# Performance work log

Hardware: AMD Instinct MI355X
Metric: run time of the kernel (lower is better)

Reference implementation:

```python
import jax, jax.numpy as jnp
from jax import lax
import numpy as np

CONF_THRESH = 0.015
NMS_DIST = 4
BORDER = 4
RED = 8


def setup_inputs() -> dict:
    key = jax.random.key(0)
    k1, k2, k3, k4, k5 = jax.random.split(key, 5)
    B, C, H, W = 32, 128, 64, 64
    MID, NCLS = 256, RED * RED + 1
    return {
        "x": jax.random.normal(k1, (B, C, H, W), dtype=jnp.float32),
        "w1": jax.random.normal(k2, (MID, C, 3, 3), dtype=jnp.float32) * 0.05,
        "b1": jax.random.normal(k3, (MID,), dtype=jnp.float32) * 0.05,
        "w2": jax.random.normal(k4, (NCLS, MID, 1, 1), dtype=jnp.float32) * 0.05,
        "b2": jax.random.normal(k5, (NCLS,), dtype=jnp.float32) * 0.05,
    }


def _conv3x3(x, w, b):
    y = lax.conv_general_dilated(
        x, w, window_strides=(1, 1), padding="SAME",
        dimension_numbers=("NCHW", "OIHW", "NCHW"))
    return y + b[None, :, None, None]


def _max_pool(s, r):
    # s: [B, H, W]; infinity-norm neighborhood max, window (2r+1)x(2r+1)
    return lax.reduce_window(
        s, -jnp.inf, lax.max,
        window_dimensions=(1, 2 * r + 1, 2 * r + 1),
        window_strides=(1, 1, 1), padding="SAME")


def _grid_nms(scores, r, iters=8):
    # Iterated local-max suppression; converges to the greedy (sorted-by-score)
    # grid NMS of the original nms_fast routine for distinct scores.
    zeros = jnp.zeros_like(scores)
    max_mask = (scores == _max_pool(scores, r)) & (scores > 0)
    for _ in range(iters):
        supp = _max_pool(max_mask.astype(scores.dtype), r) > 0
        supp_scores = jnp.where(supp, zeros, scores)
        new_max = (supp_scores == _max_pool(supp_scores, r)) & (supp_scores > 0)
        max_mask = max_mask | (new_max & ~supp)
    return jnp.where(max_mask, scores, zeros)


def reference(x, w1, b1, w2, b2):
    B, _, hh, ww = x.shape
    h = jax.nn.relu(_conv3x3(x, w1, b1))                       # [B, mid, hh, ww]
    semi = jnp.einsum("bchw,oc->bohw", h, w2[:, :, 0, 0]) + b2[None, :, None, None]
    dense = jax.nn.softmax(semi, axis=1)                        # [B, 65, hh, ww]
    nodust = dense[:, :-1]                                      # drop dust bin
    # depth-to-space: [B,64,hh,ww] -> [B, hh*8, ww*8]
    heat = nodust.transpose(0, 2, 3, 1).reshape(B, hh, ww, RED, RED)
    heat = heat.transpose(0, 1, 3, 2, 4).reshape(B, hh * RED, ww * RED)
    # confidence threshold
    scores = jnp.where(heat >= CONF_THRESH, heat, 0.0)
    # grid-based NMS (dense keep-map formulation of nms_fast)
    kept = _grid_nms(scores, NMS_DIST)
    # border removal
    Hi, Wi = hh * RED, ww * RED
    yy = jnp.arange(Hi)
    xx = jnp.arange(Wi)
    border = ((yy[:, None] >= BORDER) & (yy[:, None] < Hi - BORDER) &
              (xx[None, :] >= BORDER) & (xx[None, :] < Wi - BORDER))
    return kept * border[None, :, :].astype(kept.dtype)
```

## Files before the change

### kernel.cpp

```cpp
#include <hip/hip_runtime.h>
#include <hip/hip_bf16.h>
#include <stdint.h>

#define BATCH 32
#define CIN 128
#define HH 64
#define WW 64
#define MID 256
#define NCLS 65
#define HI 512
#define NWORDS 8
#define HBS2 264
#define SEMS 68
#define RMS 68

typedef _Float16 half8 __attribute__((ext_vector_type(8)));
typedef _Float16 half4v __attribute__((ext_vector_type(4)));
typedef _Float16 half2v __attribute__((ext_vector_type(2)));
typedef float f32x4 __attribute__((ext_vector_type(4)));

__global__ __launch_bounds__(256) void prep_w1f(
    const float* __restrict__ w1, _Float16* __restrict__ w1fh,
    _Float16* __restrict__ w1fl)
{
    const int idx = blockIdx.x * 256 + threadIdx.x;
    const int j = idx & 7, lane = (idx >> 3) & 63, mt = (idx >> 9) & 15;
    const int s = (idx >> 13) & 3, kix = idx >> 15;
    const int m = mt * 16 + (lane & 15);
    const int c = s * 32 + (lane >> 4) * 8 + j;
    const int ky = kix / 3, kx = kix - ky * 3;
    const float v = w1[((m * CIN + c) * 3 + ky) * 3 + kx];
    const _Float16 hi = (_Float16)v;
    w1fh[idx] = hi;
    w1fl[idx] = (_Float16)(v - (float)hi);
}

__global__ __launch_bounds__(256) void prep_w2f(
    const float* __restrict__ w2, _Float16* __restrict__ w2fh,
    _Float16* __restrict__ w2fl)
{
    const int idx = blockIdx.x * 256 + threadIdx.x;
    const int j = idx & 7, lane = (idx >> 3) & 63;
    const int ks = (idx >> 9) & 7, mt = idx >> 12;
    const int o = mt * 16 + (lane & 15);
    const int k = ks * 32 + (lane >> 4) * 8 + j;
    const float v = (o < NCLS) ? w2[o * MID + k] : 0.f;
    const _Float16 hi = (_Float16)v;
    w2fh[idx] = hi;
    w2fl[idx] = (_Float16)(v - (float)hi);
}

__global__ __launch_bounds__(256, 3) void head_kernel(
    const float* __restrict__ x,
    const _Float16* __restrict__ w1fh, const _Float16* __restrict__ w1fl,
    const _Float16* __restrict__ w2fh, const _Float16* __restrict__ w2fl,
    const float* __restrict__ b1, const float* __restrict__ b2,
    float* __restrict__ out)
{
    const int b  = blockIdx.z;
    const int y0 = blockIdx.y * 8, x0 = blockIdx.x * 8;
    const int tid = threadIdx.x;
    const int lane = tid & 63, w = tid >> 6;
    const int n = lane & 15, q = lane >> 4;

    __shared__ __align__(16) unsigned char SM[51200];
    char* const xhb = (char*)SM;
    _Float16* const hbh = (_Float16*)SM;
    _Float16* const hbl = hbh + 32 * HBS2;
    float* const sem  = (float*)(SM + 33792);
    float* const rinv = sem + 32 * SEMS;

    const float* xb = x + (size_t)b * CIN * HH * WW;
    for (int i = tid; i < 6400; i += 256) {
        const int c2 = i / 100, pos = i - c2 * 100;
        const int r = pos / 10, cc = pos - r * 10;
        const int gy = y0 - 1 + r, gx = x0 - 1 + cc;
        float v0 = 0.f, v1 = 0.f;
        if ((unsigned)gy < HH && (unsigned)gx < WW) {
            const float* p = xb + (c2 * 2 * HH + gy) * WW + gx;
            v0 = p[0]; v1 = p[HH * WW];
        }
        const _Float16 h0 = (_Float16)v0, h1 = (_Float16)v1;
        half2v hi = {h0, h1};
        half2v lo = {(_Float16)(v0 - (float)h0), (_Float16)(v1 - (float)h1)};
        const int slot = (c2 >> 2) ^ (pos & 15);
        char* p16 = xhb + pos * 256 + (slot << 4) + (c2 & 3) * 4;
        *(half2v*)p16 = hi;
        *(half2v*)(p16 + 25600) = lo;
    }
    __syncthreads();

    f32x4 acc[4][4];
#pragma unroll
    for (int i = 0; i < 4; ++i)
#pragma unroll
        for (int t = 0; t < 4; ++t) acc[i][t] = (f32x4){0.f, 0.f, 0.f, 0.f};

    int bposT[4];
#pragma unroll
    for (int t = 0; t < 4; ++t)
        bposT[t] = (t * 2 + (n >> 3)) * 10 + (n & 7);

    for (int kix = 0; kix < 9; ++kix) {
        const int ky = kix / 3;
        const int koff = ky * 10 + (kix - ky * 3);
#pragma unroll
        for (int s = 0; s < 4; ++s) {
            half8 Bh[4], Bl[4];
#pragma unroll
            for (int t = 0; t < 4; ++t) {
                const int pos = bposT[t] + koff;
                const int byteoff = pos * 256 +
                    ((((s << 2) + q) ^ (pos & 15)) << 4);
                Bh[t] = *(const half8*)(xhb + byteoff);
                Bl[t] = *(const half8*)(xhb + 25600 + byteoff);
            }
#pragma unroll
            for (int i = 0; i < 4; ++i) {
                const size_t o = (size_t)(kix * 4 + s) * 8192 +
                                 (w * 4 + i) * 512 + lane * 8;
                const half8 Ah = *(const half8*)(w1fh + o);
                const half8 Al = *(const half8*)(w1fl + o);
#pragma unroll
                for (int t = 0; t < 4; ++t) {
                    acc[i][t] = __builtin_amdgcn_mfma_f32_16x16x32_f16(
                        Ah, Bh[t], acc[i][t], 0, 0, 0);
                    acc[i][t] = __builtin_amdgcn_mfma_f32_16x16x32_f16(
                        Ah, Bl[t], acc[i][t], 0, 0, 0);
                    acc[i][t] = __builtin_amdgcn_mfma_f32_16x16x32_f16(
                        Al, Bh[t], acc[i][t], 0, 0, 0);
                }
            }
        }
    }
    __syncthreads();

    for (int hf = 0; hf < 2; ++hf) {
        if (hf) __syncthreads();
#pragma unroll
        for (int i = 0; i < 4; ++i)
#pragma unroll
            for (int tt = 0; tt < 2; ++tt) {
                const int t = hf * 2 + tt;
                const int p = tt * 16 + n;
                const int m0 = w * 64 + i * 16 + q * 4;
                const f32x4 a = acc[i][t];
                const float4 bv = *(const float4*)(b1 + m0);
                const float h0 = fmaxf(a[0] + bv.x, 0.f);
                const float h1 = fmaxf(a[1] + bv.y, 0.f);
                const float h2 = fmaxf(a[2] + bv.z, 0.f);
                const float h3 = fmaxf(a[3] + bv.w, 0.f);
                half4v hh = {(_Float16)h0, (_Float16)h1,
                             (_Float16)h2, (_Float16)h3};
                half4v hl = {(_Float16)(h0 - (float)hh[0]),
                             (_Float16)(h1 - (float)hh[1]),
                             (_Float16)(h2 - (float)hh[2]),
                             (_Float16)(h3 - (float)hh[3])};
                *(half4v*)(hbh + p * HBS2 + m0) = hh;
                *(half4v*)(hbl + p * HBS2 + m0) = hl;
            }
        __syncthreads();
        {
            const int nt = w & 1;
            const int mt0 = (w < 2) ? 0 : 3;
            const int nmt = (w < 2) ? 3 : 2;
            const int pb = nt * 16 + n;
            f32x4 a2[3];
#pragma unroll
            for (int j = 0; j < 3; ++j) a2[j] = (f32x4){0.f, 0.f, 0.f, 0.f};
#pragma unroll
            for (int ks = 0; ks < 8; ++ks) {
                const int ad = pb * HBS2 + ks * 32 + q * 8;
                const half8 B2h = *(const half8*)(hbh + ad);
                const half8 B2l = *(const half8*)(hbl + ad);
#pragma unroll
                for (int j = 0; j < 3; ++j)
                    if (j < nmt) {
                        const size_t o = (size_t)((mt0 + j) * 8 + ks) * 512 +
                                         lane * 8;
                        const half8 A2h = *(const half8*)(w2fh + o);
                        const half8 A2l = *(const half8*)(w2fl + o);
                        a2[j] = __builtin_amdgcn_mfma_f32_16x16x32_f16(
                            A2h, B2h, a2[j], 0, 0, 0);
                        a2[j] = __builtin_amdgcn_mfma_f32_16x16x32_f16(
                            A2h, B2l, a2[j], 0, 0, 0);
                        a2[j] = __builtin_amdgcn_mfma_f32_16x16x32_f16(
                            A2l, B2h, a2[j], 0, 0, 0);
                    }
            }
#pragma unroll
            for (int j = 0; j < 3; ++j)
                if (j < nmt) {
                    const int o0 = (mt0 + j) * 16 + q * 4;
#pragma unroll
                    for (int r2 = 0; r2 < 4; ++r2) {
                        const int o = o0 + r2;
                        if (o < NCLS)
                            sem[pb * SEMS + o] = a2[j][r2] + b2[o];
                    }
                }
        }
        __syncthreads();
        if (tid < 128) {
            const int p = tid >> 2, q4 = tid & 3;
            const int o0 = q4 * 17;
            const int o1 = (o0 + 17 < NCLS) ? o0 + 17 : NCLS;
            float mx = -1e30f;
            for (int o = o0; o < o1; ++o)
                mx = fmaxf(mx, sem[p * SEMS + o]);
            mx = fmaxf(mx, __shfl_xor(mx, 1));
            mx = fmaxf(mx, __shfl_xor(mx, 2));
            float ssum = 0.f;
            for (int o = o0; o < o1; ++o) {
                float e = __expf(sem[p * SEMS + o] - mx);
                sem[p * SEMS + o] = e;
                ssum += e;
            }
            ssum += __shfl_xor(ssum, 1);
            ssum += __shfl_xor(ssum, 2);
            if (q4 == 0) rinv[p] = 1.f / ssum;
        }
        __syncthreads();
        for (int t2 = tid; t2 < 2048; t2 += 256) {
            const int p = t2 >> 6, o = t2 & 63;
            float v = sem[p * SEMS + o] * rinv[p];
            if (!(v >= 0.015f)) v = 0.f;
            const int P = hf * 32 + p;
            const int py = P >> 3, px = P & 7;
            const int row = (y0 + py) * 8 + (o >> 3);
            const int col = (x0 + px) * 8 + (o & 7);
            out[((size_t)b * HI + row) * HI + col] = v;
        }
    }
}

__global__ __launch_bounds__(256, 8) void nms_iter(
    const float* __restrict__ S, const uint64_t* __restrict__ Min,
    uint64_t* __restrict__ Mout)
{
    const int b = blockIdx.z;
    const int bx = blockIdx.x;
    const int ty = blockIdx.y * 64, tx = bx * 64;
    const int tid = threadIdx.x;

    __shared__ uint64_t smw[80 * 3];
    __shared__ uint64_t hd[80 * 3];
    __shared__ uint64_t sup[72 * 3];
    __shared__ __align__(16) float rm[40 * RMS];

    if (tid < 240) {
        const int i = tid / 3, j = tid % 3;
        const int yy = ty - 8 + i;
        const int wj = bx - 1 + j;
        uint64_t v = 0;
        if (Min && (unsigned)yy < HI && (unsigned)wj < NWORDS)
            v = Min[((size_t)b * HI + yy) * NWORDS + wj];
        smw[tid] = v;
    }
    __syncthreads();
    if (tid < 240) {
        const int j = tid % 3;
        const uint64_t c = smw[tid];
        const uint64_t l = j > 0 ? smw[tid - 1] : 0ull;
        const uint64_t r = j < 2 ? smw[tid + 1] : 0ull;
        uint64_t d = c;
#pragma unroll
        for (int s = 1; s <= 4; ++s)
            d |= (c >> s) | (r << (64 - s)) | (c << s) | (l >> (64 - s));
        hd[tid] = d;
    }
    __syncthreads();
    if (tid < 216) {
        uint64_t v = 0;
#pragma unroll
        for (int k = 0; k < 9; ++k) v |= hd[tid + 3 * k];
        sup[tid] = v;
    }
    __syncthreads();

    const float* Sb = S + (size_t)b * HI * HI;
    for (int half = 0; half < 2; ++half) {
        const int rbase = half * 32;
        for (int k = tid; k < 640; k += 256) {
            const int rr = k >> 4, g = k & 15;
            const int r = rbase + rr;
            const int gy = ty - 4 + r;
            const int x4 = g * 4;
            const int gx0 = tx + x4 - 4;
            float v[12];
            if ((unsigned)gy < HI) {
                const float* row = Sb + (size_t)gy * HI;
                if (gx0 >= 0 && gx0 <= HI - 12) {
                    const float4 A  = *(const float4*)(row + gx0);
                    const float4 Bq = *(const float4*)(row + gx0 + 4);
                    const float4 Cq = *(const float4*)(row + gx0 + 8);
                    v[0]=A.x; v[1]=A.y; v[2]=A.z; v[3]=A.w;
                    v[4]=Bq.x; v[5]=Bq.y; v[6]=Bq.z; v[7]=Bq.w;
                    v[8]=Cq.x; v[9]=Cq.y; v[10]=Cq.z; v[11]=Cq.w;
                } else {
#pragma unroll
                    for (int cc = 0; cc < 12; ++cc)
                        v[cc] = ((unsigned)(gx0 + cc) < HI) ? row[gx0 + cc]
                                                            : 0.f;
                }
            } else {
#pragma unroll
                for (int cc = 0; cc < 12; ++cc) v[cc] = 0.f;
            }
            const uint64_t* sr = sup + r * 3;
            const uint64_t w0 = sr[(60 + x4) >> 6];
            const uint64_t w1 = sr[(64 + x4) >> 6];
            const uint64_t w2 = sr[(68 + x4) >> 6];
            const int b0 = (60 + x4) & 63;
            const int b1 = (64 + x4) & 63;
            const int b2 = (68 + x4) & 63;
#pragma unroll
            for (int cc = 0; cc < 4; ++cc) {
                if ((w0 >> (b0 + cc)) & 1ull) v[cc] = 0.f;
                if ((w1 >> (b1 + cc)) & 1ull) v[4 + cc] = 0.f;
                if ((w2 >> (b2 + cc)) & 1ull) v[8 + cc] = 0.f;
            }
            const float m4567 = fmaxf(fmaxf(v[4],v[5]), fmaxf(v[6],v[7]));
            const float m23 = fmaxf(v[2],v[3]), m89 = fmaxf(v[8],v[9]);
            const float o0 = fmaxf(fmaxf(fmaxf(v[0],v[1]), m23),
                                   fmaxf(m4567, v[8]));
            const float o1 = fmaxf(fmaxf(v[1], m23), fmaxf(m4567, m89));
            const float o2 = fmaxf(fmaxf(m23, m4567), fmaxf(m89, v[10]));
            const float o3 = fmaxf(fmaxf(v[3], m4567),
                                   fmaxf(fmaxf(m89, v[10]), v[11]));
            *(float4*)(rm + rr * RMS + x4) = make_float4(o0,o1,o2,o3);
        }
        __syncthreads();
        {
            const int wv = tid >> 6, lane = tid & 63;
            const int rb = wv * 8;
            const int ybase = rbase + rb;
            float ring[9];
#pragma unroll
            for (int k = 0; k < 8; ++k) ring[k] = rm[(rb + k) * RMS + lane];
#pragma unroll
            for (int qq = 0; qq < 8; ++qq) {
                const int y = ybase + qq;
                ring[(qq + 8) % 9] = rm[(rb + qq + 8) * RMS + lane];
                float mv = ring[0];
#pragma unroll
                for (int k = 1; k < 9; ++k) mv = fmaxf(mv, ring[k]);
                float c = Sb[(size_t)(ty + y) * HI + tx + lane];
                if ((sup[(y + 4) * 3 + 1] >> lane) & 1ull) c = 0.f;
                const uint64_t oldw = smw[(y + 8) * 3 + 1];
                const bool keep = ((oldw >> lane) & 1ull) ||
                                  (c > 0.f && c == mv);
                const uint64_t word = __ballot(keep);
                if (lane == 0)
                    Mout[((size_t)b * HI + ty + y) * NWORDS + bx] = word;
            }
        }
        __syncthreads();
    }
}

__global__ __launch_bounds__(256) void finalize_bits(
    float* __restrict__ S, const uint64_t* __restrict__ Mw)
{
    const int i4 = blockIdx.x * 256 + threadIdx.x;
    const size_t base = (size_t)i4 * 4;
    const int x = (int)(base & 511);
    const int y = (int)((base >> 9) & 511);
    const int bb = (int)(base >> 18);
    const uint64_t w = Mw[((size_t)bb * HI + y) * NWORDS + (x >> 6)];
    float4 v = ((const float4*)S)[i4];
    float* pv = (float*)&v;
    const bool rowok = (y >= 4) && (y < HI - 4);
#pragma unroll
    for (int cc = 0; cc < 4; ++cc) {
        const int xx = x + cc;
        const bool keep = rowok && (xx >= 4) && (xx < HI - 4) &&
                          ((w >> (xx & 63)) & 1ull);
        if (!keep) pv[cc] = 0.f;
    }
    ((float4*)S)[i4] = v;
}

extern "C" void kernel_launch(void* const* d_in, const int* in_sizes, int n_in,
                              void* d_out, int out_size, void* d_ws, size_t ws_size,
                              hipStream_t stream) {
    const float* x  = (const float*)d_in[0];
    const float* w1 = (const float*)d_in[1];
    const float* b1 = (const float*)d_in[2];
    const float* w2 = (const float*)d_in[3];
    const float* b2 = (const float*)d_in[4];
    float* out = (float*)d_out;

    char* wsb = (char*)d_ws;
    _Float16* w1fh = (_Float16*)(wsb);
    _Float16* w1fl = (_Float16*)(wsb + 0x90000);
    _Float16* w2fh = (_Float16*)(wsb + 0x120000);
    _Float16* w2fl = (_Float16*)(wsb + 0x130000);
    uint64_t* MA   = (uint64_t*)(wsb + 0x140000);
    uint64_t* MB   = (uint64_t*)(wsb + 0x240000);

    prep_w1f<<<294912 / 256, 256, 0, stream>>>(w1, w1fh, w1fl);
    prep_w2f<<<20480 / 256, 256, 0, stream>>>(w2, w2fh, w2fl);
    head_kernel<<<dim3(8, 8, BATCH), 256, 0, stream>>>(
        x, w1fh, w1fl, w2fh, w2fl, b1, b2, out);

    dim3 g(NWORDS, 8, BATCH);
    nms_iter<<<g, 256, 0, stream>>>(out, nullptr, MA);
    for (int it = 0; it < 4; ++it) {
        nms_iter<<<g, 256, 0, stream>>>(out, MA, MB);
        nms_iter<<<g, 256, 0, stream>>>(out, MB, MA);
    }
    const int nf4 = BATCH * HI * HI / 4;
    finalize_bits<<<nf4 / 256, 256, 0, stream>>>(out, MA);
}
```

Measured before the change: 536.0 us.

## Fuse pairs of NMS iterations per launch and fold finalize into last pass

Adds an nms_pair kernel that computes two suppression iterations per launch using an enlarged halo tile in shared memory, halving the number of NMS launches from nine to five. When workspace allows, scores are written to a workspace buffer and a new nms_last kernel applies the final iteration, the border mask and the output write together, removing the separate finalize pass. This trades extra halo recomputation and larger shared memory (lower occupancy bound) for fewer launches and less global traffic.

Result: slower. 598.8 us (+11.7%).

```diff
diff --git a/kernel.cpp b/kernel.cpp
--- a/kernel.cpp
+++ b/kernel.cpp
@@ -234,7 +234,7 @@
     }
 }
 
-__global__ __launch_bounds__(256, 8) void nms_iter(
+__global__ __launch_bounds__(256, 4) void nms_pair(
     const float* __restrict__ S, const uint64_t* __restrict__ Min,
     uint64_t* __restrict__ Mout)
 {
@@ -243,17 +243,256 @@
     const int ty = blockIdx.y * 64, tx = bx * 64;
     const int tid = threadIdx.x;
 
+    __shared__ uint64_t smw[96 * 3];
+    __shared__ uint64_t hd[96 * 3];
+    __shared__ uint64_t sup[88 * 3];
+    __shared__ uint64_t mkA[80 * 3];
+    __shared__ __align__(16) float hm[88 * 80];
+
+    const float* Sb = S + (size_t)b * HI * HI;
+
+    for (int k = tid; k < 288; k += 256) {
+        const int i = k / 3, j = k - (k / 3) * 3;
+        const int yy = ty - 16 + i;
+        const int wj = bx - 1 + j;
+        uint64_t v = 0;
+        if (Min && (unsigned)yy < HI && (unsigned)wj < NWORDS)
+            v = Min[((size_t)b * HI + yy) * NWORDS + wj];
+        smw[k] = v;
+    }
+    __syncthreads();
+    for (int k = tid; k < 288; k += 256) {
+        const int j = k % 3;
+        const uint64_t c = smw[k];
+        const uint64_t l = j > 0 ? smw[k - 1] : 0ull;
+        const uint64_t r = j < 2 ? smw[k + 1] : 0ull;
+        uint64_t d = c;
+#pragma unroll
+        for (int s = 1; s <= 4; ++s)
+            d |= (c >> s) | (r << (64 - s)) | (c << s) | (l >> (64 - s));
+        hd[k] = d;
+    }
+    __syncthreads();
+    for (int k = tid; k < 264; k += 256) {
+        uint64_t v = 0;
+#pragma unroll
+        for (int t = 0; t < 9; ++t) v |= hd[k + 3 * t];
+        sup[k] = v;
+    }
+    __syncthreads();
+    for (int k = tid; k < 1760; k += 256) {
+        const int r = k / 20, g = k - (k / 20) * 20;
+        const int gy = ty - 12 + r;
+        const int gx0 = tx - 12 + 4 * g;
+        float v[12];
+        if ((unsigned)gy < HI) {
+            const float* row = Sb + (size_t)gy * HI;
+            if (gx0 >= 0 && gx0 <= HI - 12) {
+                const float4 A  = *(const float4*)(row + gx0);
+                const float4 Bq = *(const float4*)(row + gx0 + 4);
+                const float4 Cq = *(const float4*)(row + gx0 + 8);
+                v[0]=A.x; v[1]=A.y; v[2]=A.z; v[3]=A.w;
+                v[4]=Bq.x; v[5]=Bq.y; v[6]=Bq.z; v[7]=Bq.w;
+                v[8]=Cq.x; v[9]=Cq.y; v[10]=Cq.z; v[11]=Cq.w;
+            } else {
+#pragma unroll
+                for (int cc = 0; cc < 12; ++cc)
+                    v[cc] = ((unsigned)(gx0 + cc) < HI) ? row[gx0 + cc] : 0.f;
+            }
+        } else {
+#pragma unroll
+            for (int cc = 0; cc < 12; ++cc) v[cc] = 0.f;
+        }
+        const uint64_t* sr = sup + r * 3;
+        const int rb0 = 52 + 4 * g;
+        const uint64_t w0 = sr[rb0 >> 6];
+        const uint64_t w1 = sr[(rb0 + 4) >> 6];
+        const uint64_t w2 = sr[(rb0 + 8) >> 6];
+        const int b0 = rb0 & 63, b1 = (rb0 + 4) & 63, b2 = (rb0 + 8) & 63;
+#pragma unroll
+        for (int cc = 0; cc < 4; ++cc) {
+            if ((w0 >> (b0 + cc)) & 1ull) v[cc] = 0.f;
+            if ((w1 >> (b1 + cc)) & 1ull) v[4 + cc] = 0.f;
+            if ((w2 >> (b2 + cc)) & 1ull) v[8 + cc] = 0.f;
+        }
+        const float m4567 = fmaxf(fmaxf(v[4],v[5]), fmaxf(v[6],v[7]));
+        const float m23 = fmaxf(v[2],v[3]), m89 = fmaxf(v[8],v[9]);
+        const float o0 = fmaxf(fmaxf(fmaxf(v[0],v[1]), m23),
+                               fmaxf(m4567, v[8]));
+        const float o1 = fmaxf(fmaxf(v[1], m23), fmaxf(m4567, m89));
+        const float o2 = fmaxf(fmaxf(m23, m4567), fmaxf(m89, v[10]));
+        const float o3 = fmaxf(fmaxf(v[3], m4567),
+                               fmaxf(fmaxf(m89, v[10]), v[11]));
+        *(float4*)(hm + r * 80 + 4 * g) = make_float4(o0,o1,o2,o3);
+    }
+    __syncthreads();
+    {
+        const int wv = tid >> 6, lane = tid & 63;
+        const int a0 = wv * 20;
+        float ringA[9], ringB[9];
+#pragma unroll
+        for (int t = 0; t < 8; ++t) {
+            ringA[t] = hm[(a0 + t) * 80 + lane];
+            ringB[t] = (lane < 16) ? hm[(a0 + t) * 80 + 64 + lane] : 0.f;
+        }
+        for (int ii = 0; ii < 20; ++ii) {
+            const int a = a0 + ii;
+            ringA[(ii + 8) % 9] = hm[(a + 8) * 80 + lane];
+            ringB[(ii + 8) % 9] =
+                (lane < 16) ? hm[(a + 8) * 80 + 64 + lane] : 0.f;
+            float mvA = ringA[0], mvB = ringB[0];
+#pragma unroll
+            for (int t = 1; t < 9; ++t) {
+                mvA = fmaxf(mvA, ringA[t]);
+                mvB = fmaxf(mvB, ringB[t]);
+            }
+            const int gyA = ty - 8 + a;
+            const int colA = tx - 8 + lane;
+            float cA = 0.f;
+            if ((unsigned)gyA < HI && (unsigned)colA < HI)
+                cA = Sb[(size_t)gyA * HI + colA];
+            if ((sup[(a + 4) * 3 + ((56 + lane) >> 6)] >>
+                 ((56 + lane) & 63)) & 1ull)
+                cA = 0.f;
+            const bool bitA =
+                (smw[(a + 8) * 3 + ((56 + lane) >> 6)] >>
+                 ((56 + lane) & 63)) & 1ull;
+            const bool keepA = bitA || (cA > 0.f && cA == mvA);
+            bool keepB = false;
+            if (lane < 16) {
+                const int colB = tx + 56 + lane;
+                float cB = 0.f;
+                if ((unsigned)gyA < HI && (unsigned)colB < HI)
+                    cB = Sb[(size_t)gyA * HI + colB];
+                if ((sup[(a + 4) * 3 + ((120 + lane) >> 6)] >>
+                     ((120 + lane) & 63)) & 1ull)
+                    cB = 0.f;
+                const bool bitB =
+                    (smw[(a + 8) * 3 + ((120 + lane) >> 6)] >>
+                     ((120 + lane) & 63)) & 1ull;
+                keepB = bitB || (cB > 0.f && cB == mvB);
+            }
+            const uint64_t bA = __ballot(keepA);
+            const uint64_t bB = __ballot(keepB);
+            if (lane == 0) {
+                mkA[a * 3 + 0] = (bA & 0xFFull) << 56;
+                mkA[a * 3 + 1] = (bA >> 8) | ((bB & 0xFFull) << 56);
+                mkA[a * 3 + 2] = (bB >> 8) & 0xFFull;
+            }
+        }
+    }
+    __syncthreads();
+    for (int k = tid; k < 240; k += 256) {
+        const int j = k % 3;
+        const uint64_t c = mkA[k];
+        const uint64_t l = j > 0 ? mkA[k - 1] : 0ull;
+        const uint64_t r = j < 2 ? mkA[k + 1] : 0ull;
+        uint64_t d = c;
+#pragma unroll
+        for (int s = 1; s <= 4; ++s)
+            d |= (c >> s) | (r << (64 - s)) | (c << s) | (l >> (64 - s));
+        hd[k] = d;
+    }
+    __syncthreads();
+    for (int k = tid; k < 216; k += 256) {
+        uint64_t v = 0;
+#pragma unroll
+        for (int t = 0; t < 9; ++t) v |= hd[k + 3 * t];
+        sup[k] = v;
+    }
+    __syncthreads();
+    float* const rm = hm;
+    for (int k = tid; k < 1152; k += 256) {
+        const int r = k >> 4, g = k & 15;
+        const int gy = ty - 4 + r;
+        const int gx0 = tx + 4 * g - 4;
+        float v[12];
+        if ((unsigned)gy < HI) {
+            const float* row = Sb + (size_t)gy * HI;
+            if (gx0 >= 0 && gx0 <= HI - 12) {
+                const float4 A  = *(const float4*)(row + gx0);
+                const float4 Bq = *(const float4*)(row + gx0 + 4);
+                const float4 Cq = *(const float4*)(row + gx0 + 8);
+                v[0]=A.x; v[1]=A.y; v[2]=A.z; v[3]=A.w;
+                v[4]=Bq.x; v[5]=Bq.y; v[6]=Bq.z; v[7]=Bq.w;
+                v[8]=Cq.x; v[9]=Cq.y; v[10]=Cq.z; v[11]=Cq.w;
+            } else {
+#pragma unroll
+                for (int cc = 0; cc < 12; ++cc)
+                    v[cc] = ((unsigned)(gx0 + cc) < HI) ? row[gx0 + cc] : 0.f;
+            }
+        } else {
+#pragma unroll
+            for (int cc = 0; cc < 12; ++cc) v[cc] = 0.f;
+        }
+        const uint64_t* sr = sup + r * 3;
+        const int rb0 = 60 + 4 * g;
+        const uint64_t w0 = sr[rb0 >> 6];
+        const uint64_t w1 = sr[(rb0 + 4) >> 6];
+        const uint64_t w2 = sr[(rb0 + 8) >> 6];
+        const int b0 = rb0 & 63, b1 = (rb0 + 4) & 63, b2 = (rb0 + 8) & 63;
+#pragma unroll
+        for (int cc = 0; cc < 4; ++cc) {
+            if ((w0 >> (b0 + cc)) & 1ull) v[cc] = 0.f;
+            if ((w1 >> (b1 + cc)) & 1ull) v[4 + cc] = 0.f;
+            if ((w2 >> (b2 + cc)) & 1ull) v[8 + cc] = 0.f;
+        }
+        const float m4567 = fmaxf(fmaxf(v[4],v[5]), fmaxf(v[6],v[7]));
+        const float m23 = fmaxf(v[2],v[3]), m89 = fmaxf(v[8],v[9]);
+        const float o0 = fmaxf(fmaxf(fmaxf(v[0],v[1]), m23),
+                               fmaxf(m4567, v[8]));
+        const float o1 = fmaxf(fmaxf(v[1], m23), fmaxf(m4567, m89));
+        const float o2 = fmaxf(fmaxf(m23, m4567), fmaxf(m89, v[10]));
+        const float o3 = fmaxf(fmaxf(v[3], m4567),
+                               fmaxf(fmaxf(m89, v[10]), v[11]));
+        *(float4*)(rm + r * 68 + 4 * g) = make_float4(o0,o1,o2,o3);
+    }
+    __syncthreads();
+    {
+        const int wv = tid >> 6, lane = tid & 63;
+        const int y0w = wv * 16;
+        float ring[9];
+#pragma unroll
+        for (int t = 0; t < 8; ++t) ring[t] = rm[(y0w + t) * 68 + lane];
+        for (int ii = 0; ii < 16; ++ii) {
+            const int y = y0w + ii;
+            ring[(ii + 8) % 9] = rm[(y + 8) * 68 + lane];
+            float mv = ring[0];
+#pragma unroll
+            for (int t = 1; t < 9; ++t) mv = fmaxf(mv, ring[t]);
+            float c = Sb[(size_t)(ty + y) * HI + tx + lane];
+            if ((sup[(y + 4) * 3 + 1] >> lane) & 1ull) c = 0.f;
+            const bool old = (mkA[(y + 8) * 3 + 1] >> lane) & 1ull;
+            const bool keep = old || (c > 0.f && c == mv);
+            const uint64_t word = __ballot(keep);
+            if (lane == 0)
+                Mout[((size_t)b * HI + ty + y) * NWORDS + bx] = word;
+        }
+    }
+}
+
+__global__ __launch_bounds__(256, 8) void nms_last(
+    const float* __restrict__ S, const uint64_t* __restrict__ Min,
+    float* __restrict__ out)
+{
+    const int b = blockIdx.z;
+    const int bx = blockIdx.x;
+    const int ty = blockIdx.y * 64, tx = bx * 64;
+    const int tid = threadIdx.x;
+
     __shared__ uint64_t smw[80 * 3];
     __shared__ uint64_t hd[80 * 3];
     __shared__ uint64_t sup[72 * 3];
     __shared__ __align__(16) float rm[40 * RMS];
+
+    const float* Sb = S + (size_t)b * HI * HI;
 
     if (tid < 240) {
         const int i = tid / 3, j = tid % 3;
         const int yy = ty - 8 + i;
         const int wj = bx - 1 + j;
         uint64_t v = 0;
-        if (Min && (unsigned)yy < HI && (unsigned)wj < NWORDS)
+        if ((unsigned)yy < HI && (unsigned)wj < NWORDS)
             v = Min[((size_t)b * HI + yy) * NWORDS + wj];
         smw[tid] = v;
     }
@@ -278,7 +517,6 @@
     }
     __syncthreads();
 
-    const float* Sb = S + (size_t)b * HI * HI;
     for (int half = 0; half < 2; ++half) {
         const int rbase = half * 32;
         for (int k = tid; k < 640; k += 256) {
@@ -345,6 +583,135 @@
                 float mv = ring[0];
 #pragma unroll
                 for (int k = 1; k < 9; ++k) mv = fmaxf(mv, ring[k]);
+                const int gy = ty + y, gx = tx + lane;
+                const float corig = Sb[(size_t)gy * HI + gx];
+                float c = corig;
+                if ((sup[(y + 4) * 3 + 1] >> lane) & 1ull) c = 0.f;
+                const uint64_t oldw = smw[(y + 8) * 3 + 1];
+                const bool keep = ((oldw >> lane) & 1ull) ||
+                                  (c > 0.f && c == mv);
+                const bool border = (gy >= 4) && (gy < HI - 4) &&
+                                    (gx >= 4) && (gx < HI - 4);
+                out[((size_t)b * HI + gy) * HI + gx] =
+                    (keep && border) ? corig : 0.f;
+            }
+        }
+        __syncthreads();
+    }
+}
+
+__global__ __launch_bounds__(256, 8) void nms_iter(
+    const float* __restrict__ S, const uint64_t* __restrict__ Min,
+    uint64_t* __restrict__ Mout)
+{
+    const int b = blockIdx.z;
+    const int bx = blockIdx.x;
+    const int ty = blockIdx.y * 64, tx = bx * 64;
+    const int tid = threadIdx.x;
+
+    __shared__ uint64_t smw[80 * 3];
+    __shared__ uint64_t hd[80 * 3];
+    __shared__ uint64_t sup[72 * 3];
+    __shared__ __align__(16) float rm[40 * RMS];
+
+    const float* Sb = S + (size_t)b * HI * HI;
+
+    if (tid < 240) {
+        const int i = tid / 3, j = tid % 3;
+        const int yy = ty - 8 + i;
+        const int wj = bx - 1 + j;
+        uint64_t v = 0;
+        if (Min && (unsigned)yy < HI && (unsigned)wj < NWORDS)
+            v = Min[((size_t)b * HI + yy) * NWORDS + wj];
+        smw[tid] = v;
+    }
+    __syncthreads();
+    if (tid < 240) {
+        const int j = tid % 3;
+        const uint64_t c = smw[tid];
+        const uint64_t l = j > 0 ? smw[tid - 1] : 0ull;
+        const uint64_t r = j < 2 ? smw[tid + 1] : 0ull;
+        uint64_t d = c;
+#pragma unroll
+        for (int s = 1; s <= 4; ++s)
+            d |= (c >> s) | (r << (64 - s)) | (c << s) | (l >> (64 - s));
+        hd[tid] = d;
+    }
+    __syncthreads();
+    if (tid < 216) {
+        uint64_t v = 0;
+#pragma unroll
+        for (int k = 0; k < 9; ++k) v |= hd[tid + 3 * k];
+        sup[tid] = v;
+    }
+    __syncthreads();
+
+    for (int half = 0; half < 2; ++half) {
+        const int rbase = half * 32;
+        for (int k = tid; k < 640; k += 256) {
+            const int rr = k >> 4, g = k & 15;
+            const int r = rbase + rr;
+            const int gy = ty - 4 + r;
+            const int x4 = g * 4;
+            const int gx0 = tx + x4 - 4;
+            float v[12];
+            if ((unsigned)gy < HI) {
+                const float* row = Sb + (size_t)gy * HI;
+                if (gx0 >= 0 && gx0 <= HI - 12) {
+                    const float4 A  = *(const float4*)(row + gx0);
+                    const float4 Bq = *(const float4*)(row + gx0 + 4);
+                    const float4 Cq = *(const float4*)(row + gx0 + 8);
+                    v[0]=A.x; v[1]=A.y; v[2]=A.z; v[3]=A.w;
+                    v[4]=Bq.x; v[5]=Bq.y; v[6]=Bq.z; v[7]=Bq.w;
+                    v[8]=Cq.x; v[9]=Cq.y; v[10]=Cq.z; v[11]=Cq.w;
+                } else {
+#pragma unroll
+                    for (int cc = 0; cc < 12; ++cc)
+                        v[cc] = ((unsigned)(gx0 + cc) < HI) ? row[gx0 + cc]
+                                                            : 0.f;
+                }
+            } else {
+#pragma unroll
+                for (int cc = 0; cc < 12; ++cc) v[cc] = 0.f;
+            }
+            const uint64_t* sr = sup + r * 3;
+            const uint64_t w0 = sr[(60 + x4) >> 6];
+            const uint64_t w1 = sr[(64 + x4) >> 6];
+            const uint64_t w2 = sr[(68 + x4) >> 6];
+            const int b0 = (60 + x4) & 63;
+            const int b1 = (64 + x4) & 63;
+            const int b2 = (68 + x4) & 63;
+#pragma unroll
+            for (int cc = 0; cc < 4; ++cc) {
+                if ((w0 >> (b0 + cc)) & 1ull) v[cc] = 0.f;
+                if ((w1 >> (b1 + cc)) & 1ull) v[4 + cc] = 0.f;
+                if ((w2 >> (b2 + cc)) & 1ull) v[8 + cc] = 0.f;
+            }
+            const float m4567 = fmaxf(fmaxf(v[4],v[5]), fmaxf(v[6],v[7]));
+            const float m23 = fmaxf(v[2],v[3]), m89 = fmaxf(v[8],v[9]);
+            const float o0 = fmaxf(fmaxf(fmaxf(v[0],v[1]), m23),
+                                   fmaxf(m4567, v[8]));
+            const float o1 = fmaxf(fmaxf(v[1], m23), fmaxf(m4567, m89));
+            const float o2 = fmaxf(fmaxf(m23, m4567), fmaxf(m89, v[10]));
+            const float o3 = fmaxf(fmaxf(v[3], m4567),
+                                   fmaxf(fmaxf(m89, v[10]), v[11]));
+            *(float4*)(rm + rr * RMS + x4) = make_float4(o0,o1,o2,o3);
+        }
+        __syncthreads();
+        {
+            const int wv = tid >> 6, lane = tid & 63;
+            const int rb = wv * 8;
+            const int ybase = rbase + rb;
+            float ring[9];
+#pragma unroll
+            for (int k = 0; k < 8; ++k) ring[k] = rm[(rb + k) * RMS + lane];
+#pragma unroll
+            for (int qq = 0; qq < 8; ++qq) {
+                const int y = ybase + qq;
+                ring[(qq + 8) % 9] = rm[(rb + qq + 8) * RMS + lane];
+                float mv = ring[0];
+#pragma unroll
+                for (int k = 1; k < 9; ++k) mv = fmaxf(mv, ring[k]);
                 float c = Sb[(size_t)(ty + y) * HI + tx + lane];
                 if ((sup[(y + 4) * 3 + 1] >> lane) & 1ull) c = 0.f;
                 const uint64_t oldw = smw[(y + 8) * 3 + 1];
@@ -399,17 +766,27 @@
     uint64_t* MA   = (uint64_t*)(wsb + 0x140000);
     uint64_t* MB   = (uint64_t*)(wsb + 0x240000);
 
+    const size_t S_OFF = 0x340000;
+    const size_t S_BYTES = (size_t)BATCH * HI * HI * 4;
+    const bool use_ws = ws_size >= S_OFF + S_BYTES;
+    float* S = use_ws ? (float*)(wsb + S_OFF) : out;
+
     prep_w1f<<<294912 / 256, 256, 0, stream>>>(w1, w1fh, w1fl);
     prep_w2f<<<20480 / 256, 256, 0, stream>>>(w2, w2fh, w2fl);
     head_kernel<<<dim3(8, 8, BATCH), 256, 0, stream>>>(
-        x, w1fh, w1fl, w2fh, w2fl, b1, b2, out);
+        x, w1fh, w1fl, w2fh, w2fl, b1, b2, S);
 
     dim3 g(NWORDS, 8, BATCH);
-    nms_iter<<<g, 256, 0, stream>>>(out, nullptr, MA);
-    for (int it = 0; it < 4; ++it) {
-        nms_iter<<<g, 256, 0, stream>>>(out, MA, MB);
-        nms_iter<<<g, 256, 0, stream>>>(out, MB, MA);
-    }
-    const int nf4 = BATCH * HI * HI / 4;
-    finalize_bits<<<nf4 / 256, 256, 0, stream>>>(out, MA);
+    nms_pair<<<g, 256, 0, stream>>>(S, nullptr, MA);
+    nms_pair<<<g, 256, 0, stream>>>(S, MA, MB);
+    nms_pair<<<g, 256, 0, stream>>>(S, MB, MA);
+    nms_pair<<<g, 256, 0, stream>>>(S, MA, MB);
+
+    if (use_ws) {
+        nms_last<<<g, 256, 0, stream>>>(S, MB, out);
+    } else {
+        nms_iter<<<g, 256, 0, stream>>>(S, MB, MA);
+        const int nf4 = BATCH * HI * HI / 4;
+        finalize_bits<<<nf4 / 256, 256, 0, stream>>>(out, MA);
+    }
 }
```

## Fuse final NMS pass with border/finalize, merge weight prep kernels

Applied to the files above, without the earlier changes.

Merges the two weight-prep kernels into one launch. When the workspace is large enough, the head writes scores to a workspace buffer, and a new nms_last kernel runs the final suppression iteration and writes the masked, border-cleared scores straight to the output. This removes the separate finalize_bits pass over the full score map. The first NMS iteration also skips building the dilation bitmaps when there is no input mask. The cost is extra workspace use and a duplicated kernel body.

Result: faster. 524.1 us (-2.2%).

```diff
diff --git a/kernel.cpp b/kernel.cpp
--- a/kernel.cpp
+++ b/kernel.cpp
@@ -19,35 +19,33 @@
 typedef _Float16 half2v __attribute__((ext_vector_type(2)));
 typedef float f32x4 __attribute__((ext_vector_type(4)));
 
-__global__ __launch_bounds__(256) void prep_w1f(
-    const float* __restrict__ w1, _Float16* __restrict__ w1fh,
-    _Float16* __restrict__ w1fl)
+__global__ __launch_bounds__(256) void prep_wf(
+    const float* __restrict__ w1, const float* __restrict__ w2,
+    _Float16* __restrict__ w1fh, _Float16* __restrict__ w1fl,
+    _Float16* __restrict__ w2fh, _Float16* __restrict__ w2fl)
 {
     const int idx = blockIdx.x * 256 + threadIdx.x;
-    const int j = idx & 7, lane = (idx >> 3) & 63, mt = (idx >> 9) & 15;
-    const int s = (idx >> 13) & 3, kix = idx >> 15;
-    const int m = mt * 16 + (lane & 15);
-    const int c = s * 32 + (lane >> 4) * 8 + j;
-    const int ky = kix / 3, kx = kix - ky * 3;
-    const float v = w1[((m * CIN + c) * 3 + ky) * 3 + kx];
-    const _Float16 hi = (_Float16)v;
-    w1fh[idx] = hi;
-    w1fl[idx] = (_Float16)(v - (float)hi);
-}
-
-__global__ __launch_bounds__(256) void prep_w2f(
-    const float* __restrict__ w2, _Float16* __restrict__ w2fh,
-    _Float16* __restrict__ w2fl)
-{
-    const int idx = blockIdx.x * 256 + threadIdx.x;
-    const int j = idx & 7, lane = (idx >> 3) & 63;
-    const int ks = (idx >> 9) & 7, mt = idx >> 12;
-    const int o = mt * 16 + (lane & 15);
-    const int k = ks * 32 + (lane >> 4) * 8 + j;
-    const float v = (o < NCLS) ? w2[o * MID + k] : 0.f;
-    const _Float16 hi = (_Float16)v;
-    w2fh[idx] = hi;
-    w2fl[idx] = (_Float16)(v - (float)hi);
+    if (idx < 294912) {
+        const int j = idx & 7, lane = (idx >> 3) & 63, mt = (idx >> 9) & 15;
+        const int s = (idx >> 13) & 3, kix = idx >> 15;
+        const int m = mt * 16 + (lane & 15);
+        const int c = s * 32 + (lane >> 4) * 8 + j;
+        const int ky = kix / 3, kx = kix - ky * 3;
+        const float v = w1[((m * CIN + c) * 3 + ky) * 3 + kx];
+        const _Float16 hi = (_Float16)v;
+        w1fh[idx] = hi;
+        w1fl[idx] = (_Float16)(v - (float)hi);
+    } else {
+        const int i2 = idx - 294912;
+        const int j = i2 & 7, lane = (i2 >> 3) & 63;
+        const int ks = (i2 >> 9) & 7, mt = i2 >> 12;
+        const int o = mt * 16 + (lane & 15);
+        const int k = ks * 32 + (lane >> 4) * 8 + j;
+        const float v = (o < NCLS) ? w2[o * MID + k] : 0.f;
+        const _Float16 hi = (_Float16)v;
+        w2fh[i2] = hi;
+        w2fl[i2] = (_Float16)(v - (float)hi);
+    }
 }
 
 __global__ __launch_bounds__(256, 3) void head_kernel(
@@ -248,37 +246,44 @@
     __shared__ uint64_t sup[72 * 3];
     __shared__ __align__(16) float rm[40 * RMS];
 
-    if (tid < 240) {
-        const int i = tid / 3, j = tid % 3;
-        const int yy = ty - 8 + i;
-        const int wj = bx - 1 + j;
-        uint64_t v = 0;
-        if (Min && (unsigned)yy < HI && (unsigned)wj < NWORDS)
-            v = Min[((size_t)b * HI + yy) * NWORDS + wj];
-        smw[tid] = v;
-    }
-    __syncthreads();
-    if (tid < 240) {
-        const int j = tid % 3;
-        const uint64_t c = smw[tid];
-        const uint64_t l = j > 0 ? smw[tid - 1] : 0ull;
-        const uint64_t r = j < 2 ? smw[tid + 1] : 0ull;
-        uint64_t d = c;
-#pragma unroll
-        for (int s = 1; s <= 4; ++s)
-            d |= (c >> s) | (r << (64 - s)) | (c << s) | (l >> (64 - s));
-        hd[tid] = d;
-    }
-    __syncthreads();
-    if (tid < 216) {
-        uint64_t v = 0;
-#pragma unroll
-        for (int k = 0; k < 9; ++k) v |= hd[tid + 3 * k];
-        sup[tid] = v;
-    }
-    __syncthreads();
-
     const float* Sb = S + (size_t)b * HI * HI;
+
+    if (Min) {
+        if (tid < 240) {
+            const int i = tid / 3, j = tid % 3;
+            const int yy = ty - 8 + i;
+            const int wj = bx - 1 + j;
+            uint64_t v = 0;
+            if ((unsigned)yy < HI && (unsigned)wj < NWORDS)
+                v = Min[((size_t)b * HI + yy) * NWORDS + wj];
+            smw[tid] = v;
+        }
+        __syncthreads();
+        if (tid < 240) {
+            const int j = tid % 3;
+            const uint64_t c = smw[tid];
+            const uint64_t l = j > 0 ? smw[tid - 1] : 0ull;
+            const uint64_t r = j < 2 ? smw[tid + 1] : 0ull;
+            uint64_t d = c;
+#pragma unroll
+            for (int s = 1; s <= 4; ++s)
+                d |= (c >> s) | (r << (64 - s)) | (c << s) | (l >> (64 - s));
+            hd[tid] = d;
+        }
+        __syncthreads();
+        if (tid < 216) {
+            uint64_t v = 0;
+#pragma unroll
+            for (int k = 0; k < 9; ++k) v |= hd[tid + 3 * k];
+            sup[tid] = v;
+        }
+        __syncthreads();
+    } else {
+        if (tid < 240) smw[tid] = 0;
+        if (tid < 216) sup[tid] = 0;
+        __syncthreads();
+    }
+
     for (int half = 0; half < 2; ++half) {
         const int rbase = half * 32;
         for (int k = tid; k < 640; k += 256) {
@@ -359,6 +364,135 @@
     }
 }
 
+__global__ __launch_bounds__(256, 8) void nms_last(
+    const float* __restrict__ S, const uint64_t* __restrict__ Min,
+    float* __restrict__ out)
+{
+    const int b = blockIdx.z;
+    const int bx = blockIdx.x;
+    const int ty = blockIdx.y * 64, tx = bx * 64;
+    const int tid = threadIdx.x;
+
+    __shared__ uint64_t smw[80 * 3];
+    __shared__ uint64_t hd[80 * 3];
+    __shared__ uint64_t sup[72 * 3];
+    __shared__ __align__(16) float rm[40 * RMS];
+
+    const float* Sb = S + (size_t)b * HI * HI;
+
+    if (tid < 240) {
+        const int i = tid / 3, j = tid % 3;
+        const int yy = ty - 8 + i;
+        const int wj = bx - 1 + j;
+        uint64_t v = 0;
+        if ((unsigned)yy < HI && (unsigned)wj < NWORDS)
+            v = Min[((size_t)b * HI + yy) * NWORDS + wj];
+        smw[tid] = v;
+    }
+    __syncthreads();
+    if (tid < 240) {
+        const int j = tid % 3;
+        const uint64_t c = smw[tid];
+        const uint64_t l = j > 0 ? smw[tid - 1] : 0ull;
+        const uint64_t r = j < 2 ? smw[tid + 1] : 0ull;
+        uint64_t d = c;
+#pragma unroll
+        for (int s = 1; s <= 4; ++s)
+            d |= (c >> s) | (r << (64 - s)) | (c << s) | (l >> (64 - s));
+        hd[tid] = d;
+    }
+    __syncthreads();
+    if (tid < 216) {
+        uint64_t v = 0;
+#pragma unroll
+        for (int k = 0; k < 9; ++k) v |= hd[tid + 3 * k];
+        sup[tid] = v;
+    }
+    __syncthreads();
+
+    for (int half = 0; half < 2; ++half) {
+        const int rbase = half * 32;
+        for (int k = tid; k < 640; k += 256) {
+            const int rr = k >> 4, g = k & 15;
+            const int r = rbase + rr;
+            const int gy = ty - 4 + r;
+            const int x4 = g * 4;
+            const int gx0 = tx + x4 - 4;
+            float v[12];
+            if ((unsigned)gy < HI) {
+                const float* row = Sb + (size_t)gy * HI;
+                if (gx0 >= 0 && gx0 <= HI - 12) {
+                    const float4 A  = *(const float4*)(row + gx0);
+                    const float4 Bq = *(const float4*)(row + gx0 + 4);
+                    const float4 Cq = *(const float4*)(row + gx0 + 8);
+                    v[0]=A.x; v[1]=A.y; v[2]=A.z; v[3]=A.w;
+                    v[4]=Bq.x; v[5]=Bq.y; v[6]=Bq.z; v[7]=Bq.w;
+                    v[8]=Cq.x; v[9]=Cq.y; v[10]=Cq.z; v[11]=Cq.w;
+                } else {
+#pragma unroll
+                    for (int cc = 0; cc < 12; ++cc)
+                        v[cc] = ((unsigned)(gx0 + cc) < HI) ? row[gx0 + cc]
+                                                            : 0.f;
+                }
+            } else {
+#pragma unroll
+                for (int cc = 0; cc < 12; ++cc) v[cc] = 0.f;
+            }
+            const uint64_t* sr = sup + r * 3;
+            const uint64_t w0 = sr[(60 + x4) >> 6];
+            const uint64_t w1 = sr[(64 + x4) >> 6];
+            const uint64_t w2 = sr[(68 + x4) >> 6];
+            const int b0 = (60 + x4) & 63;
+            const int b1 = (64 + x4) & 63;
+            const int b2 = (68 + x4) & 63;
+#pragma unroll
+            for (int cc = 0; cc < 4; ++cc) {
+                if ((w0 >> (b0 + cc)) & 1ull) v[cc] = 0.f;
+                if ((w1 >> (b1 + cc)) & 1ull) v[4 + cc] = 0.f;
+                if ((w2 >> (b2 + cc)) & 1ull) v[8 + cc] = 0.f;
+            }
+            const float m4567 = fmaxf(fmaxf(v[4],v[5]), fmaxf(v[6],v[7]));
+            const float m23 = fmaxf(v[2],v[3]), m89 = fmaxf(v[8],v[9]);
+            const float o0 = fmaxf(fmaxf(fmaxf(v[0],v[1]), m23),
+                                   fmaxf(m4567, v[8]));
+            const float o1 = fmaxf(fmaxf(v[1], m23), fmaxf(m4567, m89));
+            const float o2 = fmaxf(fmaxf(m23, m4567), fmaxf(m89, v[10]));
+            const float o3 = fmaxf(fmaxf(v[3], m4567),
+                                   fmaxf(fmaxf(m89, v[10]), v[11]));
+            *(float4*)(rm + rr * RMS + x4) = make_float4(o0,o1,o2,o3);
+        }
+        __syncthreads();
+        {
+            const int wv = tid >> 6, lane = tid & 63;
+            const int rb = wv * 8;
+            const int ybase = rbase + rb;
+            float ring[9];
+#pragma unroll
+            for (int k = 0; k < 8; ++k) ring[k] = rm[(rb + k) * RMS + lane];
+#pragma unroll
+            for (int qq = 0; qq < 8; ++qq) {
+                const int y = ybase + qq;
+                ring[(qq + 8) % 9] = rm[(rb + qq + 8) * RMS + lane];
+                float mv = ring[0];
+#pragma unroll
+                for (int k = 1; k < 9; ++k) mv = fmaxf(mv, ring[k]);
+                const int gy = ty + y, gx = tx + lane;
+                const float corig = Sb[(size_t)gy * HI + gx];
+                float c = corig;
+                if ((sup[(y + 4) * 3 + 1] >> lane) & 1ull) c = 0.f;
+                const uint64_t oldw = smw[(y + 8) * 3 + 1];
+                const bool keep = ((oldw >> lane) & 1ull) ||
+                                  (c > 0.f && c == mv);
+                const bool border = (gy >= 4) && (gy < HI - 4) &&
+                                    (gx >= 4) && (gx < HI - 4);
+                out[((size_t)b * HI + gy) * HI + gx] =
+                    (keep && border) ? corig : 0.f;
+            }
+        }
+        __syncthreads();
+    }
+}
+
 __global__ __launch_bounds__(256) void finalize_bits(
     float* __restrict__ S, const uint64_t* __restrict__ Mw)
 {
@@ -399,17 +533,30 @@
     uint64_t* MA   = (uint64_t*)(wsb + 0x140000);
     uint64_t* MB   = (uint64_t*)(wsb + 0x240000);
 
-    prep_w1f<<<294912 / 256, 256, 0, stream>>>(w1, w1fh, w1fl);
-    prep_w2f<<<20480 / 256, 256, 0, stream>>>(w2, w2fh, w2fl);
+    const size_t S_OFF = 0x340000;
+    const size_t S_BYTES = (size_t)BATCH * HI * HI * 4;
+    const bool use_ws = ws_size >= S_OFF + S_BYTES;
+    float* S = use_ws ? (float*)(wsb + S_OFF) : out;
+
+    prep_wf<<<1232, 256, 0, stream>>>(w1, w2, w1fh, w1fl, w2fh, w2fl);
     head_kernel<<<dim3(8, 8, BATCH), 256, 0, stream>>>(
-        x, w1fh, w1fl, w2fh, w2fl, b1, b2, out);
+        x, w1fh, w1fl, w2fh, w2fl, b1, b2, S);
 
     dim3 g(NWORDS, 8, BATCH);
-    nms_iter<<<g, 256, 0, stream>>>(out, nullptr, MA);
-    for (int it = 0; it < 4; ++it) {
-        nms_iter<<<g, 256, 0, stream>>>(out, MA, MB);
-        nms_iter<<<g, 256, 0, stream>>>(out, MB, MA);
-    }
-    const int nf4 = BATCH * HI * HI / 4;
-    finalize_bits<<<nf4 / 256, 256, 0, stream>>>(out, MA);
+    nms_iter<<<g, 256, 0, stream>>>(S, nullptr, MA);
+    nms_iter<<<g, 256, 0, stream>>>(S, MA, MB);
+    nms_iter<<<g, 256, 0, stream>>>(S, MB, MA);
+    nms_iter<<<g, 256, 0, stream>>>(S, MA, MB);
+    nms_iter<<<g, 256, 0, stream>>>(S, MB, MA);
+    nms_iter<<<g, 256, 0, stream>>>(S, MA, MB);
+    nms_iter<<<g, 256, 0, stream>>>(S, MB, MA);
+    nms_iter<<<g, 256, 0, stream>>>(S, MA, MB);
+
+    if (use_ws) {
+        nms_last<<<g, 256, 0, stream>>>(S, MB, out);
+    } else {
+        nms_iter<<<g, 256, 0, stream>>>(S, MB, MA);
+        const int nf4 = BATCH * HI * HI / 4;
+        finalize_bits<<<nf4 / 256, 256, 0, stream>>>(out, MA);
+    }
 }
```
